# Kernel optimization log

Measured on AMD Instinct MI355X. Metric: run time of the kernel, lower is better.

Reference implementation:

```python
import jax, jax.numpy as jnp
import numpy as np

B, T, C = 4, 2048, 768
H, KVH, D = 6, 6, 128
HALF = D // 2


def setup_inputs() -> dict:
    key = jax.random.key(0)
    ks = jax.random.split(key, 5)
    x = jax.random.normal(ks[0], (B, T, C), dtype=jnp.float32)
    # true rotary frequencies
    inv_freq = 1.0 / (10000.0 ** (jnp.arange(HALF, dtype=jnp.float32) / HALF))
    ang = jnp.arange(T, dtype=jnp.float32)[:, None] * inv_freq[None, :]  # [T, HALF]
    cos, sin = jnp.cos(ang), jnp.sin(ang)
    s = 0.02
    wq = jax.random.normal(ks[1], (H * D, C), dtype=jnp.float32) * s
    wk = jax.random.normal(ks[2], (KVH * D, C), dtype=jnp.float32) * s
    wv = jax.random.normal(ks[3], (KVH * D, C), dtype=jnp.float32) * s
    wproj = jax.random.normal(ks[4], (C, C), dtype=jnp.float32) * s
    return {"x": x, "cos": cos, "sin": sin, "wq": wq, "wk": wk, "wv": wv, "wproj": wproj}


def _norm(t, eps=1e-6):
    # torch: (x - mean) / (std + eps), std unbiased (ddof=1)
    mean = jnp.mean(t, axis=-1, keepdims=True)
    var = jnp.sum((t - mean) ** 2, axis=-1, keepdims=True) / (t.shape[-1] - 1)
    return (t - mean) / (jnp.sqrt(var) + eps)


def _rope(t, cos, sin):
    # t: [B, T, heads, D]; cos/sin: [T, HALF]
    x1, x2 = t[..., :HALF], t[..., HALF:]
    c = cos[None, :, None, :]
    s = sin[None, :, None, :]
    return jnp.concatenate([x1 * c + x2 * s, -x1 * s + x2 * c], axis=-1)


def reference(x, cos, sin, wq, wk, wv, wproj):
    q = jnp.einsum('btc,oc->bto', x, wq).reshape(B, T, H, D)
    k = jnp.einsum('btc,oc->bto', x, wk).reshape(B, T, KVH, D)
    v = jnp.einsum('btc,oc->bto', x, wv).reshape(B, T, KVH, D)
    q = _norm(_rope(q, cos, sin))
    k = _norm(_rope(k, cos, sin))
    # -> [B, heads, T, D]
    q = q.transpose(0, 2, 1, 3)
    k = k.transpose(0, 2, 1, 3)
    v = v.transpose(0, 2, 1, 3)
    # nrep = H // KVH == 1, repeat_kv is a no-op here
    scale = 1.0 / jnp.sqrt(jnp.float32(D))
    scores = jnp.einsum('bhtd,bhsd->bhts', q, k) * scale  # [B,H,T,T]
    causal = jnp.tril(jnp.ones((T, T), dtype=bool))
    scores = jnp.where(causal[None, None], scores, jnp.float32(-1e30))
    attn = jax.nn.softmax(scores, axis=-1)
    y = jnp.einsum('bhts,bhsd->bhtd', attn, v)
    y = y.transpose(0, 2, 1, 3).reshape(B, T, H * D)
    return jnp.einsum('bto,co->btc', y, wproj)
```

## Files before the change

### kernel.cpp

```cpp
#include <hip/hip_runtime.h>

#define BB 4
#define TT 2048
#define CC 768
#define HH 6
#define DD 128
#define BT (BB * TT)
#define HALF 64
#define NBH (BB * HH)
#define QKSCALE 0.12753785627919282f

typedef __bf16 v8bf __attribute__((ext_vector_type(8)));
typedef float f32x4 __attribute__((ext_vector_type(4)));

__device__ __forceinline__ unsigned short f2b(float f) {
  union { float f; unsigned u; } v; v.f = f;
  unsigned r = v.u + 0x7FFFu + ((v.u >> 16) & 1u);
  return (unsigned short)(r >> 16);
}
__device__ __forceinline__ float b2f(unsigned short u) {
  union { unsigned u; float f; } v; v.u = (unsigned)u << 16;
  return v.f;
}
__device__ __forceinline__ unsigned pk2(float f0, float f1) {
  union { float f; unsigned u; } a, b; a.f = f1; b.f = f0;
  return __builtin_amdgcn_perm(a.u, b.u, 0x07060302u);
}

__device__ __forceinline__ void load_lds16(const void* g, void* l) {
  __builtin_amdgcn_global_load_lds(
      (const __attribute__((address_space(1))) unsigned int*)g,
      (__attribute__((address_space(3))) unsigned int*)(unsigned int)(unsigned long long)(l),
      16, 0, 0);
}

__global__ __launch_bounds__(256) void cvt_all_kernel(const float* __restrict__ x,
                                                      const float* __restrict__ w0,
                                                      const float* __restrict__ w1,
                                                      const float* __restrict__ w2,
                                                      const float* __restrict__ w3,
                                                      unsigned short* __restrict__ xb,
                                                      unsigned short* __restrict__ wb) {
  int bx = blockIdx.x;
  const float* src;
  unsigned short* dst;
  int i;
  if (bx < 6144) {
    src = x; dst = xb; i = bx * 256 + threadIdx.x;
  } else {
    int bsel = (bx - 6144) / 576;
    src = bsel == 0 ? w0 : bsel == 1 ? w1 : bsel == 2 ? w2 : w3;
    dst = wb + bsel * 589824;
    i = ((bx - 6144) % 576) * 256 + threadIdx.x;
  }
  float4 f = ((const float4*)src)[i];
  ushort4 o;
  o.x = f2b(f.x); o.y = f2b(f.y); o.z = f2b(f.z); o.w = f2b(f.w);
  ((ushort4*)dst)[i] = o;
}

__global__ __launch_bounds__(256) void gemm_qkv(const unsigned short* __restrict__ A,
                                                const unsigned short* __restrict__ Wall,
                                                unsigned short* __restrict__ qb,
                                                unsigned short* __restrict__ kb,
                                                unsigned short* __restrict__ vt) {
  __shared__ __align__(16) unsigned short As[2][512 * 8];
  __shared__ __align__(16) unsigned short Bs[2][512 * 8];
  const int m0 = blockIdx.x * 128;
  const int wsel = blockIdx.y / HH, h = blockIdx.y % HH;
  const unsigned short* W = Wall + (size_t)wsel * 589824 + (size_t)h * 128 * CC;
  const int tid = threadIdx.x;
  const int wave = tid >> 6, lane = tid & 63;
  const int fr = lane & 15, quad = lane >> 4;
  const int wm = (wave & 1) * 64, wn = (wave >> 1) * 64;

  f32x4 acc[4][4];
#pragma unroll
  for (int i = 0; i < 4; i++)
#pragma unroll
    for (int j = 0; j < 4; j++) acc[i][j] = (f32x4){0.f, 0.f, 0.f, 0.f};

  auto stage = [&](int kk, int buf) {
#pragma unroll
    for (int it = 0; it < 2; it++) {
      int base_slot = wave * 128 + it * 64;
      int sigma = base_slot + lane;
      int r = sigma >> 2, g = (sigma & 3) ^ ((r >> 1) & 3);
      load_lds16(A + (size_t)(m0 + r) * CC + kk + g * 8, &As[buf][base_slot * 8]);
      load_lds16(W + (size_t)r * CC + kk + g * 8, &Bs[buf][base_slot * 8]);
    }
  };

  stage(0, 0);
  __syncthreads();
  for (int step = 0; step < CC / 32; step++) {
    int buf = step & 1;
    if (step + 1 < CC / 32) stage((step + 1) * 32, buf ^ 1);
    v8bf af[4], bfr[4];
#pragma unroll
    for (int i = 0; i < 4; i++) {
      int ra = wm + i * 16 + fr;
      af[i] = *(const v8bf*)&As[buf][(4 * ra + (quad ^ ((ra >> 1) & 3))) * 8];
      int rb = wn + i * 16 + fr;
      bfr[i] = *(const v8bf*)&Bs[buf][(4 * rb + (quad ^ ((rb >> 1) & 3))) * 8];
    }
#pragma unroll
    for (int i = 0; i < 4; i++)
#pragma unroll
      for (int j = 0; j < 4; j++)
        acc[i][j] = __builtin_amdgcn_mfma_f32_16x16x32_bf16(af[i], bfr[j], acc[i][j], 0, 0, 0);
    __syncthreads();
  }

  if (wsel < 2) {
    unsigned short* dst = wsel ? kb : qb;
#pragma unroll
    for (int i = 0; i < 4; i++) {
      int rr0 = m0 + wm + i * 16 + quad * 4;
      int b = rr0 >> 11, t0 = rr0 & 2047;
      size_t base = ((size_t)(b * HH + h) * TT + t0) * DD;
#pragma unroll
      for (int j = 0; j < 4; j++) {
        int d = wn + j * 16 + fr;
#pragma unroll
        for (int r = 0; r < 4; r++)
          dst[base + (size_t)r * DD + d] = f2b(acc[i][j][r]);
      }
    }
  } else {
#pragma unroll
    for (int i = 0; i < 4; i++) {
      int rr0 = m0 + wm + i * 16 + quad * 4;
      int b = rr0 >> 11, t0 = rr0 & 2047;
      int bh = b * HH + h;
#pragma unroll
      for (int j = 0; j < 4; j++) {
        int d = wn + j * 16 + fr;
        ushort4 u = { f2b(acc[i][j][0]), f2b(acc[i][j][1]),
                      f2b(acc[i][j][2]), f2b(acc[i][j][3]) };
        *(ushort4*)&vt[((size_t)bh * DD + d) * TT + t0] = u;
      }
    }
  }
}

__global__ __launch_bounds__(256) void gemm_w64(const unsigned short* __restrict__ A,
                                                const unsigned short* __restrict__ W,
                                                float* __restrict__ C) {
  __shared__ __align__(16) unsigned short As[2][256 * 8];
  __shared__ __align__(16) unsigned short Bs[2][512 * 8];
  const int m0 = blockIdx.x * 64, n0 = blockIdx.y * 128;
  const int tid = threadIdx.x;
  const int wave = tid >> 6, lane = tid & 63;
  const int fr = lane & 15, quad = lane >> 4;
  const int wm = (wave & 1) * 32, wn = (wave >> 1) * 64;

  f32x4 acc[2][4];
#pragma unroll
  for (int i = 0; i < 2; i++)
#pragma unroll
    for (int j = 0; j < 4; j++) acc[i][j] = (f32x4){0.f, 0.f, 0.f, 0.f};

  auto stage = [&](int kk, int buf) {
    {
      int base_slot = wave * 64;
      int sigma = base_slot + lane;
      int r = sigma >> 2, g = (sigma & 3) ^ ((r >> 1) & 3);
      load_lds16(A + (size_t)(m0 + r) * CC + kk + g * 8, &As[buf][base_slot * 8]);
    }
#pragma unroll
    for (int it = 0; it < 2; it++) {
      int base_slot = wave * 128 + it * 64;
      int sigma = base_slot + lane;
      int r = sigma >> 2, g = (sigma & 3) ^ ((r >> 1) & 3);
      load_lds16(W + (size_t)(n0 + r) * CC + kk + g * 8, &Bs[buf][base_slot * 8]);
    }
  };

  stage(0, 0);
  __syncthreads();
  for (int step = 0; step < CC / 32; step++) {
    int buf = step & 1;
    if (step + 1 < CC / 32) stage((step + 1) * 32, buf ^ 1);
    v8bf af[2], bfr[4];
#pragma unroll
    for (int i = 0; i < 2; i++) {
      int ra = wm + i * 16 + fr;
      af[i] = *(const v8bf*)&As[buf][(4 * ra + (quad ^ ((ra >> 1) & 3))) * 8];
    }
#pragma unroll
    for (int j = 0; j < 4; j++) {
      int rb = wn + j * 16 + fr;
      bfr[j] = *(const v8bf*)&Bs[buf][(4 * rb + (quad ^ ((rb >> 1) & 3))) * 8];
    }
#pragma unroll
    for (int i = 0; i < 2; i++)
#pragma unroll
      for (int j = 0; j < 4; j++)
        acc[i][j] = __builtin_amdgcn_mfma_f32_16x16x32_bf16(af[i], bfr[j], acc[i][j], 0, 0, 0);
    __syncthreads();
  }

  const int orow = m0 + wm + quad * 4;
#pragma unroll
  for (int i = 0; i < 2; i++)
#pragma unroll
    for (int j = 0; j < 4; j++) {
      int oc = n0 + wn + j * 16 + fr;
#pragma unroll
      for (int r = 0; r < 4; r++)
        C[(size_t)(orow + i * 16 + r) * CC + oc] = acc[i][j][r];
    }
}

__global__ __launch_bounds__(256) void rope_all_kernel(unsigned short* __restrict__ qb,
                                                       unsigned short* __restrict__ kb,
                                                       const float* __restrict__ cosb,
                                                       const float* __restrict__ sinb) {
  int bx = blockIdx.x;
  unsigned short* qk = (bx < 12288) ? qb : kb;
  float scale = (bx < 12288) ? QKSCALE : 1.0f;
  int idx = (bx % 12288) * 4 + (threadIdx.x >> 6);
  int lane = threadIdx.x & 63;
  int tpos = idx & (TT - 1);
  size_t base = (size_t)idx * DD;

  float x1 = b2f(qk[base + lane]);
  float x2 = b2f(qk[base + HALF + lane]);
  float c = cosb[tpos * HALF + lane];
  float s = sinb[tpos * HALF + lane];
  float o1 = x1 * c + x2 * s;
  float o2 = x2 * c - x1 * s;

  float sum = o1 + o2;
#pragma unroll
  for (int off = 32; off; off >>= 1) sum += __shfl_xor(sum, off);
  float mean = sum * (1.f / 128.f);
  float d1 = o1 - mean, d2 = o2 - mean;
  float vs = d1 * d1 + d2 * d2;
#pragma unroll
  for (int off = 32; off; off >>= 1) vs += __shfl_xor(vs, off);
  float inv = scale / (sqrtf(vs * (1.f / 127.f)) + 1e-6f);

  qk[base + lane] = f2b(d1 * inv);
  qk[base + HALF + lane] = f2b(d2 * inv);
}

__global__ __launch_bounds__(256) void attn_mfma(const unsigned short* __restrict__ qtb,
                                                 const unsigned short* __restrict__ ktb,
                                                 const unsigned short* __restrict__ vtb,
                                                 unsigned short* __restrict__ Opart,
                                                 float* __restrict__ lpart) {
  __shared__ __align__(16) unsigned short Ks[2][512 * 8];
  __shared__ __align__(16) unsigned short Vts[2][512 * 8];

  const int u = blockIdx.x;
  const int bh = u % NBH;
  const int uu = u / NBH;
  int qb, c;
  if (uu < 25)       { c = 0; qb = 31 - uu; }
  else if (uu < 42)  { c = 1; qb = 31 - (uu - 25); }
  else if (uu < 51)  { c = 2; qb = 31 - (uu - 42); }
  else if (uu == 51) { c = 3; qb = 31; }
  else { int uu2 = uu - 52; int sidx = uu2 >> 2; c = uu2 & 3; qb = 8 * c + 6 - sidx; }
  const int t0 = c * 16;
  const int t1 = min(t0 + 16, 2 * qb + 2);
  const int niter = t1 - t0;

  const int tid = threadIdx.x;
  const int wave = tid >> 6, lane = tid & 63;
  const int fr = lane & 15, quad = lane >> 4;
  const int idxf = 4 * ((quad & 1) * 32 + fr);
  const int idxs = idxf + 64;
  const size_t head_base = (size_t)bh * TT * DD;
  const int m0 = qb * 64 + wave * 16;

  v8bf qf[4];
#pragma unroll
  for (int kbk = 0; kbk < 4; kbk++)
    qf[kbk] = *(const v8bf*)(qtb + head_base +
                             (size_t)(m0 + fr) * DD + kbk * 32 + quad * 8);

  const __bf16 one_bf = (__bf16)1.0f;
  v8bf ones = {one_bf, one_bf, one_bf, one_bf, one_bf, one_bf, one_bf, one_bf};

  f32x4 oacc[8];
#pragma unroll
  for (int i = 0; i < 8; i++) oacc[i] = (f32x4){0.f, 0.f, 0.f, 0.f};
  f32x4 lacc = (f32x4){0.f, 0.f, 0.f, 0.f};

  auto stage = [&](int jt, int buf) {
    const unsigned short* kbase = ktb + head_base + (size_t)(jt * 32) * DD;
    const unsigned short* vbase = vtb + head_base + jt * 32;
#pragma unroll
    for (int it = 0; it < 2; it++) {
      int base_slot = it * 256 + wave * 64;
      int sigma = base_slot + lane;
      int s = sigma >> 4, gk = (sigma & 15) ^ (s & 7);
      load_lds16(kbase + (size_t)s * DD + gk * 8, &Ks[buf][base_slot * 8]);
      int d = sigma >> 2, gv = (sigma & 3) ^ ((d >> 1) & 3);
      load_lds16(vbase + (size_t)d * TT + gv * 8, &Vts[buf][base_slot * 8]);
    }
  };

  stage(t0, 0);
  __syncthreads();

  for (int it = 0; it < niter; it++) {
    const int jt = t0 + it;
    const int buf = it & 1;
    if (it + 1 < niter) stage(jt + 1, buf ^ 1);

    const int j0 = jt * 32;
    if (j0 <= m0 + 15) {
      f32x4 st0 = (f32x4){0.f, 0.f, 0.f, 0.f};
      f32x4 st1 = (f32x4){0.f, 0.f, 0.f, 0.f};
      __builtin_amdgcn_s_setprio(1);
#pragma unroll
      for (int kbk = 0; kbk < 4; kbk++) {
        int g = 4 * kbk + quad;
        int gx = (g ^ (fr & 7)) * 8;
        v8bf a0 = *(const v8bf*)&Ks[buf][(16 * fr) * 8 + gx];
        v8bf a1 = *(const v8bf*)&Ks[buf][(16 * (fr + 16)) * 8 + gx];
        st0 = __builtin_amdgcn_mfma_f32_16x16x32_bf16(a0, qf[kbk], st0, 0, 0, 0);
        st1 = __builtin_amdgcn_mfma_f32_16x16x32_bf16(a1, qf[kbk], st1, 0, 0, 0);
      }
      __builtin_amdgcn_s_setprio(0);

      const bool diag = (j0 + 31 > m0);
      float p[8];
      if (diag) {
        const int qrow = m0 + fr;
#pragma unroll
        for (int r = 0; r < 4; r++) {
          int c0 = j0 + quad * 4 + r;
          p[r]     = (c0      <= qrow) ? exp2f(st0[r]) : 0.f;
          p[4 + r] = (c0 + 16 <= qrow) ? exp2f(st1[r]) : 0.f;
        }
      } else {
#pragma unroll
        for (int r = 0; r < 4; r++) { p[r] = exp2f(st0[r]); p[4 + r] = exp2f(st1[r]); }
      }
      unsigned A0 = pk2(p[0], p[1]), A1 = pk2(p[2], p[3]);
      unsigned B0 = pk2(p[4], p[5]), B1 = pk2(p[6], p[7]);
      unsigned alo0 = (unsigned)__builtin_amdgcn_ds_bpermute(idxf, (int)A0);
      unsigned alo1 = (unsigned)__builtin_amdgcn_ds_bpermute(idxf, (int)A1);
      unsigned ahi0 = (unsigned)__builtin_amdgcn_ds_bpermute(idxs, (int)A0);
      unsigned ahi1 = (unsigned)__builtin_amdgcn_ds_bpermute(idxs, (int)A1);
      unsigned blo0 = (unsigned)__builtin_amdgcn_ds_bpermute(idxf, (int)B0);
      unsigned blo1 = (unsigned)__builtin_amdgcn_ds_bpermute(idxf, (int)B1);
      unsigned bhi0 = (unsigned)__builtin_amdgcn_ds_bpermute(idxs, (int)B0);
      unsigned bhi1 = (unsigned)__builtin_amdgcn_ds_bpermute(idxs, (int)B1);
      const bool ql = (quad < 2);
      union { unsigned w[4]; v8bf v; } pw;
      pw.w[0] = ql ? alo0 : blo0;
      pw.w[1] = ql ? alo1 : blo1;
      pw.w[2] = ql ? ahi0 : bhi0;
      pw.w[3] = ql ? ahi1 : bhi1;
      v8bf pa = pw.v;

      __builtin_amdgcn_s_setprio(1);
#pragma unroll
      for (int nt2 = 0; nt2 < 8; nt2++) {
        int d = nt2 * 16 + fr;
        v8bf vb = *(const v8bf*)&Vts[buf][(4 * d + (quad ^ ((d >> 1) & 3))) * 8];
        oacc[nt2] = __builtin_amdgcn_mfma_f32_16x16x32_bf16(pa, vb, oacc[nt2], 0, 0, 0);
      }
      lacc = __builtin_amdgcn_mfma_f32_16x16x32_bf16(pa, ones, lacc, 0, 0, 0);
      __builtin_amdgcn_s_setprio(0);
    }
    __syncthreads();
  }

  unsigned short* Oc = Opart + (size_t)c * (NBH * TT * DD) + head_base;
#pragma unroll
  for (int nt2 = 0; nt2 < 8; nt2++)
#pragma unroll
    for (int r = 0; r < 4; r++)
      Oc[(size_t)(m0 + quad * 4 + r) * DD + nt2 * 16 + fr] = f2b(oacc[nt2][r]);
  if (fr == 0) {
#pragma unroll
    for (int r = 0; r < 4; r++)
      lpart[c * (NBH * TT) + bh * TT + m0 + quad * 4 + r] = lacc[r];
  }
}

__global__ __launch_bounds__(256) void combine_kernel(const unsigned short* __restrict__ Opart,
                                                      const float* __restrict__ lpart,
                                                      unsigned short* __restrict__ yb) {
  int idx = blockIdx.x * 256 + threadIdx.x;
  int row = idx >> 5;
  int dg = (idx & 31) * 4;
  int t = row & 2047;
  int qt = t >> 7;
  int nc = (4 * qt + 4 + 15) >> 4;

  float a0 = 0.f, a1 = 0.f, a2 = 0.f, a3 = 0.f, l = 0.f;
  for (int cchunk = 0; cchunk < nc; cchunk++) {
    ushort4 o = *(const ushort4*)&Opart[(size_t)cchunk * (NBH * TT * DD) + (size_t)row * DD + dg];
    a0 += b2f(o.x); a1 += b2f(o.y); a2 += b2f(o.z); a3 += b2f(o.w);
    l += lpart[cchunk * (NBH * TT) + row];
  }
  float linv = 1.f / l;
  int bh = row >> 11;
  int b = bh / HH, h = bh % HH;
  ushort4 uo = { f2b(a0 * linv), f2b(a1 * linv), f2b(a2 * linv), f2b(a3 * linv) };
  *(ushort4*)&yb[((size_t)(b * TT + t)) * CC + h * DD + dg] = uo;
}

extern "C" void kernel_launch(void* const* d_in, const int* in_sizes, int n_in,
                              void* d_out, int out_size, void* d_ws, size_t ws_size,
                              hipStream_t stream) {
  const float* x     = (const float*)d_in[0];
  const float* cosb  = (const float*)d_in[1];
  const float* sinb  = (const float*)d_in[2];
  const float* wq    = (const float*)d_in[3];
  const float* wk    = (const float*)d_in[4];
  const float* wv    = (const float*)d_in[5];
  const float* wproj = (const float*)d_in[6];
  float* out = (float*)d_out;

  char* w = (char*)d_ws;
  unsigned short* q_t   = (unsigned short*)(w);
  unsigned short* k_t   = (unsigned short*)(w + 12582912);
  unsigned short* v_t   = (unsigned short*)(w + 25165824);
  unsigned short* yb    = (unsigned short*)(w + 37748736);
  unsigned short* xb    = (unsigned short*)(w + 50331648);
  float*          lpart = (float*)(w + 50331648);
  unsigned short* wb    = (unsigned short*)(w + 62914560);
  unsigned short* Opart = (unsigned short*)(w + 67633152);

  cvt_all_kernel<<<8448, 256, 0, stream>>>(x, wq, wk, wv, wproj, xb, wb);

  gemm_qkv<<<dim3(BT / 128, 3 * HH), 256, 0, stream>>>(xb, wb, q_t, k_t, v_t);

  rope_all_kernel<<<24576, 256, 0, stream>>>(q_t, k_t, cosb, sinb);

  attn_mfma<<<1920, 256, 0, stream>>>(q_t, k_t, v_t, Opart, lpart);
  combine_kernel<<<6144, 256, 0, stream>>>(Opart, lpart, yb);

  gemm_w64<<<dim3(BT / 64, CC / 128), 256, 0, stream>>>(yb, wb + 3 * 589824, out);
}
```

Before: 243.7 us.

## Load V fragments directly from global memory into registers, bypass LDS

Removes the LDS staging buffer for transposed V. Each wave now loads its V operand fragments straight from global memory into registers at the start of each tile, issued before the QK^T MFMAs so the latency can overlap with them. K keeps the double-buffered LDS path, with its precomputed swizzled offsets hoisted out of the loop. exp2f is replaced by raw v_exp_f32 inline asm. This cuts LDS traffic and footprint, which may allow more blocks per CU. In exchange, all four waves redundantly fetch the same V data from global/L2, and the loads may not be fully hidden before the PV MFMAs need them.

```diff
diff --git a/kernel.cpp b/kernel.cpp
--- a/kernel.cpp
+++ b/kernel.cpp
@@ -25,6 +25,9 @@
 __device__ __forceinline__ unsigned pk2(float f0, float f1) {
   union { float f; unsigned u; } a, b; a.f = f1; b.f = f0;
   return __builtin_amdgcn_perm(a.u, b.u, 0x07060302u);
+}
+__device__ __forceinline__ float ex2(float x) {
+  float r; asm("v_exp_f32 %0, %1" : "=v"(r) : "v"(x)); return r;
 }
 
 __device__ __forceinline__ void load_lds16(const void* g, void* l) {
@@ -252,7 +255,6 @@
                                                  unsigned short* __restrict__ Opart,
                                                  float* __restrict__ lpart) {
   __shared__ __align__(16) unsigned short Ks[2][512 * 8];
-  __shared__ __align__(16) unsigned short Vts[2][512 * 8];
 
   const int u = blockIdx.x;
   const int bh = u % NBH;
@@ -289,30 +291,43 @@
   for (int i = 0; i < 8; i++) oacc[i] = (f32x4){0.f, 0.f, 0.f, 0.f};
   f32x4 lacc = (f32x4){0.f, 0.f, 0.f, 0.f};
 
-  auto stage = [&](int jt, int buf) {
-    const unsigned short* kbase = ktb + head_base + (size_t)(jt * 32) * DD;
-    const unsigned short* vbase = vtb + head_base + jt * 32;
-#pragma unroll
-    for (int it = 0; it < 2; it++) {
-      int base_slot = it * 256 + wave * 64;
-      int sigma = base_slot + lane;
-      int s = sigma >> 4, gk = (sigma & 15) ^ (s & 7);
-      load_lds16(kbase + (size_t)s * DD + gk * 8, &Ks[buf][base_slot * 8]);
-      int d = sigma >> 2, gv = (sigma & 3) ^ ((d >> 1) & 3);
-      load_lds16(vbase + (size_t)d * TT + gv * 8, &Vts[buf][base_slot * 8]);
-    }
+  const unsigned short* khead = ktb + head_base;
+  int sg0 = wave * 64 + lane;
+  int sg1 = 256 + wave * 64 + lane;
+  const int kg0 = (sg0 >> 4) * DD + (((sg0 & 15) ^ ((sg0 >> 4) & 7)) * 8);
+  const int kg1 = (sg1 >> 4) * DD + (((sg1 & 15) ^ ((sg1 >> 4) & 7)) * 8);
+  unsigned short* ks0a = &Ks[0][sg0 * 8];
+  unsigned short* ks1a = &Ks[0][sg1 * 8];
+  unsigned short* ks0b = &Ks[1][sg0 * 8];
+  unsigned short* ks1b = &Ks[1][sg1 * 8];
+
+  const unsigned short* vhead = vtb + head_base;
+  const unsigned vbase0 = (unsigned)(fr * TT + t0 * 32 + quad * 8);
+
+  auto stageK = [&](int jt, int buf) {
+    const unsigned short* kb2 = khead + (size_t)(jt * 32) * DD;
+    load_lds16(kb2 + kg0, buf ? ks0b : ks0a);
+    load_lds16(kb2 + kg1, buf ? ks1b : ks1a);
   };
 
-  stage(t0, 0);
+  stageK(t0, 0);
   __syncthreads();
 
   for (int it = 0; it < niter; it++) {
     const int jt = t0 + it;
     const int buf = it & 1;
-    if (it + 1 < niter) stage(jt + 1, buf ^ 1);
+    if (it + 1 < niter) stageK(jt + 1, buf ^ 1);
 
     const int j0 = jt * 32;
     if (j0 <= m0 + 15) {
+      v8bf vf[8];
+      {
+        const unsigned vo = vbase0 + (unsigned)(it * 32);
+#pragma unroll
+        for (int nt2 = 0; nt2 < 8; nt2++)
+          vf[nt2] = *(const v8bf*)&vhead[vo + (unsigned)(nt2 * 16 * TT)];
+      }
+
       f32x4 st0 = (f32x4){0.f, 0.f, 0.f, 0.f};
       f32x4 st1 = (f32x4){0.f, 0.f, 0.f, 0.f};
       __builtin_amdgcn_s_setprio(1);
@@ -334,12 +349,12 @@
 #pragma unroll
         for (int r = 0; r < 4; r++) {
           int c0 = j0 + quad * 4 + r;
-          p[r]     = (c0      <= qrow) ? exp2f(st0[r]) : 0.f;
-          p[4 + r] = (c0 + 16 <= qrow) ? exp2f(st1[r]) : 0.f;
+          p[r]     = (c0      <= qrow) ? ex2(st0[r]) : 0.f;
+          p[4 + r] = (c0 + 16 <= qrow) ? ex2(st1[r]) : 0.f;
         }
       } else {
 #pragma unroll
-        for (int r = 0; r < 4; r++) { p[r] = exp2f(st0[r]); p[4 + r] = exp2f(st1[r]); }
+        for (int r = 0; r < 4; r++) { p[r] = ex2(st0[r]); p[4 + r] = ex2(st1[r]); }
       }
       unsigned A0 = pk2(p[0], p[1]), A1 = pk2(p[2], p[3]);
       unsigned B0 = pk2(p[4], p[5]), B1 = pk2(p[6], p[7]);
@@ -361,11 +376,8 @@
 
       __builtin_amdgcn_s_setprio(1);
 #pragma unroll
-      for (int nt2 = 0; nt2 < 8; nt2++) {
-        int d = nt2 * 16 + fr;
-        v8bf vb = *(const v8bf*)&Vts[buf][(4 * d + (quad ^ ((d >> 1) & 3))) * 8];
-        oacc[nt2] = __builtin_amdgcn_mfma_f32_16x16x32_bf16(pa, vb, oacc[nt2], 0, 0, 0);
-      }
+      for (int nt2 = 0; nt2 < 8; nt2++)
+        oacc[nt2] = __builtin_amdgcn_mfma_f32_16x16x32_bf16(pa, vf[nt2], oacc[nt2], 0, 0, 0);
       lacc = __builtin_amdgcn_mfma_f32_16x16x32_bf16(pa, ones, lacc, 0, 0, 0);
       __builtin_amdgcn_s_setprio(0);
     }
```

After: 291.5 us. 1.2x slower.
